# Performance work log

Hardware: AMD Instinct MI355X
Metric: run time of the kernel (lower is better)

## Reference

```python
import jax, jax.numpy as jnp
import numpy as np

N_NODES = 100000
N_EDGES = 640000
D_IN = 128
D_OUT = 128


def setup_inputs() -> dict:
    key = jax.random.key(0)
    k1, k2, k3, k4, k5, k6 = jax.random.split(key, 6)
    x = jax.random.normal(k1, (N_NODES, D_IN), dtype=jnp.float32)
    edge_weights = jax.random.uniform(k2, (N_EDGES, 1), dtype=jnp.float32)
    src = jax.random.randint(k3, (N_EDGES,), 0, N_NODES)
    dst = jax.random.randint(k4, (N_EDGES,), 0, N_NODES)
    # nn.Linear init scale ~ 1/sqrt(in_feats)
    W = jax.random.normal(k5, (D_OUT, D_IN), dtype=jnp.float32) / np.sqrt(D_IN)
    b = jax.random.normal(k6, (D_OUT,), dtype=jnp.float32) / np.sqrt(D_IN)
    return {"x": x, "edge_weights": edge_weights, "src": src, "dst": dst, "W": W, "b": b}


def reference(x, edge_weights, src, dst, W, b):
    # message: gather source node features, scale by per-edge weight  [E, D]
    m = x[src] * edge_weights
    # reduce: sum messages into destination nodes  [N, D]
    h = jax.ops.segment_sum(m, dst, num_segments=N_NODES)
    # dense linear  [N, D_OUT]
    return h @ W.T + b
```

## Files before the change

kernel.cpp:

```cpp
#include <hip/hip_runtime.h>
#include <hip/hip_bf16.h>

#define D 128
#define SCAN_CH 4096
#define HIST_BLOCKS 512

typedef __bf16 bf16x8 __attribute__((ext_vector_type(8)));
typedef float  f32x4  __attribute__((ext_vector_type(4)));
typedef float  f32x2  __attribute__((ext_vector_type(2)));

__device__ __forceinline__ __bf16 f2bf(float f) { return (__bf16)f; }
__device__ __forceinline__ int pad8(int v) { return (v + 7) & ~7; }

__global__ __launch_bounds__(256) void prep_kernel(
    const float* __restrict__ W, __bf16* __restrict__ wb,
    int* __restrict__ cnt, int M, int4* __restrict__ bins4, long nbin4)
{
    long t    = (long)blockIdx.x * 256 + threadIdx.x;
    long nthr = (long)gridDim.x * 256;

    for (long i = t; i < nbin4; i += nthr) bins4[i] = make_int4(0, 0, 0, 0);
    for (long i = t; i < M; i += nthr) cnt[i] = 0;

    if (t < 2048) {
        int lane = (int)t & 63;
        int frag = (int)t >> 6;
        int kb = frag >> 3, fn = frag & 7;
        int n  = fn * 16 + (lane & 15);
        int k0 = kb * 32 + (lane >> 4) * 8;
        const float* src = &W[(size_t)n * D + k0];
        float4 v0 = *reinterpret_cast<const float4*>(src);
        float4 v1 = *reinterpret_cast<const float4*>(src + 4);
        bf16x8 o;
        o[0]=f2bf(v0.x); o[1]=f2bf(v0.y); o[2]=f2bf(v0.z); o[3]=f2bf(v0.w);
        o[4]=f2bf(v1.x); o[5]=f2bf(v1.y); o[6]=f2bf(v1.z); o[7]=f2bf(v1.w);
        *reinterpret_cast<bf16x8*>(&wb[((size_t)frag * 64 + lane) * 8]) = o;
    }
}

__global__ __launch_bounds__(256) void gemm_hist_kernel(
    const float* __restrict__ x, const __bf16* __restrict__ wb,
    __bf16* __restrict__ y, int M,
    const int* __restrict__ dst, int* __restrict__ cnt,
    int* __restrict__ rank, int E)
{
    const int tid = threadIdx.x;

    if (blockIdx.x < HIST_BLOCKS) {
        int t    = blockIdx.x * 256 + tid;
        int nthr = HIST_BLOCKS * 256;
        for (int e = t; e < E; e += nthr) {
            int d = dst[e];
            rank[e] = atomicAdd(&cnt[d], 1);
        }
        return;
    }

    const int gb   = blockIdx.x - HIST_BLOCKS;
    const int lane = tid & 63;
    const int wv   = tid >> 6;
    const int l15  = lane & 15;
    const int l4   = lane >> 4;
    const int row_base = gb * 128 + wv * 32;
    if (row_base >= M) return;

    f32x4 av[2][8];
    #pragma unroll
    for (int mi = 0; mi < 2; ++mi) {
        int row = row_base + mi * 16 + l15;
        int rc  = row < M ? row : M - 1;
        const f32x4* ap = reinterpret_cast<const f32x4*>(&x[(size_t)rc * D + l4 * 8]);
        #pragma unroll
        for (int kb = 0; kb < 4; ++kb) {
            av[mi][kb * 2]     = __builtin_nontemporal_load(ap + kb * 8);
            av[mi][kb * 2 + 1] = __builtin_nontemporal_load(ap + kb * 8 + 1);
        }
    }

    f32x4 acc[2][8];
    #pragma unroll
    for (int mi = 0; mi < 2; ++mi)
        #pragma unroll
        for (int fn = 0; fn < 8; ++fn)
            #pragma unroll
            for (int c = 0; c < 4; ++c) acc[mi][fn][c] = 0.f;

    #pragma unroll
    for (int kb = 0; kb < 4; ++kb) {
        bf16x8 b[8];
        #pragma unroll
        for (int fn = 0; fn < 8; ++fn)
            b[fn] = *reinterpret_cast<const bf16x8*>(
                        &wb[((size_t)(kb * 8 + fn) * 64 + lane) * 8]);
        #pragma unroll
        for (int mi = 0; mi < 2; ++mi) {
            f32x4 v0 = av[mi][kb * 2];
            f32x4 v1 = av[mi][kb * 2 + 1];
            bf16x8 a;
            a[0]=f2bf(v0[0]); a[1]=f2bf(v0[1]); a[2]=f2bf(v0[2]); a[3]=f2bf(v0[3]);
            a[4]=f2bf(v1[0]); a[5]=f2bf(v1[1]); a[6]=f2bf(v1[2]); a[7]=f2bf(v1[3]);
            #pragma unroll
            for (int fn = 0; fn < 8; ++fn)
                acc[mi][fn] = __builtin_amdgcn_mfma_f32_16x16x32_bf16(
                                  a, b[fn], acc[mi][fn], 0, 0, 0);
        }
    }

    #pragma unroll
    for (int mi = 0; mi < 2; ++mi)
        #pragma unroll
        for (int r = 0; r < 4; ++r) {
            int row = row_base + mi * 16 + l4 * 4 + r;
            if (row >= M) continue;
            #pragma unroll
            for (int fn = 0; fn < 8; ++fn)
                y[(size_t)row * D + fn * 16 + l15] = f2bf(acc[mi][fn][r]);
        }
}

__global__ __launch_bounds__(256) void scan_part_kernel(
    const int* __restrict__ cnt, int* __restrict__ bsum, int N)
{
    __shared__ int wred[4];
    const int tid  = threadIdx.x;
    const int lane = tid & 63;
    const int wid  = tid >> 6;
    int off = blockIdx.x * SCAN_CH + tid * 16;
    int s = 0;
    #pragma unroll
    for (int i = 0; i < 16; ++i) {
        int idx = off + i;
        if (idx < N) s += pad8(cnt[idx]);
    }
    #pragma unroll
    for (int d = 32; d >= 1; d >>= 1) s += __shfl_xor(s, d, 64);
    if (lane == 0) wred[wid] = s;
    __syncthreads();
    if (tid == 0) bsum[blockIdx.x] = wred[0] + wred[1] + wred[2] + wred[3];
}

__global__ __launch_bounds__(256) void scan_write_kernel(
    const int* __restrict__ cnt, const int* __restrict__ bsum,
    int* __restrict__ base, int N, int NB)
{
    __shared__ int boff_s;
    __shared__ int wsum[4];
    const int b    = blockIdx.x;
    const int tid  = threadIdx.x;
    const int lane = tid & 63;
    const int wid  = tid >> 6;

    if (wid == 0) {
        int v = (lane < b) ? bsum[lane] : 0;
        #pragma unroll
        for (int d = 32; d >= 1; d >>= 1) v += __shfl_xor(v, d, 64);
        if (lane == 0) boff_s = v;
    }
    __syncthreads();

    int off = b * SCAN_CH + tid * 16;
    int v[16];
    int s = 0;
    #pragma unroll
    for (int i = 0; i < 16; ++i) {
        int idx = off + i;
        v[i] = (idx < N) ? pad8(cnt[idx]) : 0;
        s += v[i];
    }
    int ssum = s;
    #pragma unroll
    for (int d = 1; d < 64; d <<= 1) {
        int t = __shfl_up(ssum, d, 64);
        if (lane >= d) ssum += t;
    }
    if (lane == 63) wsum[wid] = ssum;
    __syncthreads();
    int woff = 0;
    for (int w = 0; w < wid; ++w) woff += wsum[w];

    int run = boff_s + woff + ssum - s;
    #pragma unroll
    for (int i = 0; i < 16; ++i) {
        int idx = off + i;
        if (idx < N) base[idx] = run;
        if (idx == N - 1) base[N] = run + v[i];
        run += v[i];
    }
}

__global__ __launch_bounds__(256) void bin_kernel(
    const int* __restrict__ src, const int* __restrict__ dst,
    const float* __restrict__ ew, const int* __restrict__ base,
    const int* __restrict__ rank, int2* __restrict__ bins, int E)
{
    int e = blockIdx.x * 256 + threadIdx.x;
    if (e >= E) return;
    int d  = __builtin_nontemporal_load(&dst[e]);
    int sv = __builtin_nontemporal_load(&src[e]);
    float w = __builtin_nontemporal_load(&ew[e]);
    int rk = __builtin_nontemporal_load(&rank[e]);
    int p = base[d] + rk;
    bins[p] = make_int2(sv * (D / 2), __float_as_int(w));
}

__global__ __launch_bounds__(256) void gather_kernel(
    const __bf16* __restrict__ y, const int* __restrict__ base,
    const int2* __restrict__ bins, const float* __restrict__ bias,
    float* __restrict__ out, int N)
{
    int gw   = (blockIdx.x * 256 + threadIdx.x) >> 6;
    int lane = threadIdx.x & 63;
    if (gw >= N) return;

    const unsigned* yb = reinterpret_cast<const unsigned*>(y);
    const int b0 = __builtin_amdgcn_readfirstlane(base[gw]);
    const int b1 = __builtin_amdgcn_readfirstlane(base[gw + 1]);
    float accx = 0.f, accy = 0.f;

    for (int i = b0; i < b1; i += 8) {
        int2 e[8];
        #pragma unroll
        for (int t = 0; t < 8; ++t) e[t] = bins[i + t];
        unsigned p[8];
        #pragma unroll
        for (int t = 0; t < 8; ++t)
            p[t] = yb[(unsigned)e[t].x + lane];
        #pragma unroll
        for (int t = 0; t < 8; ++t) {
            float w = __int_as_float(e[t].y);
            accx += __uint_as_float(p[t] << 16) * w;
            accy += __uint_as_float(p[t] & 0xFFFF0000u) * w;
        }
    }

    float2 bv = *reinterpret_cast<const float2*>(&bias[lane * 2]);
    f32x2 o;
    o[0] = accx + bv.x;
    o[1] = accy + bv.y;
    __builtin_nontemporal_store(o, reinterpret_cast<f32x2*>(&out[(size_t)gw * D + lane * 2]));
}

extern "C" void kernel_launch(void* const* d_in, const int* in_sizes, int n_in,
                              void* d_out, int out_size, void* d_ws, size_t ws_size,
                              hipStream_t stream) {
    const float* x   = (const float*)d_in[0];
    const float* ew  = (const float*)d_in[1];
    const int*   src = (const int*)d_in[2];
    const int*   dst = (const int*)d_in[3];
    const float* W   = (const float*)d_in[4];
    const float* b   = (const float*)d_in[5];
    float*       out = (float*)d_out;

    const int E  = in_sizes[2];
    const int M  = out_size / D;
    const int NB = (M + SCAN_CH - 1) / SCAN_CH;
    const size_t BIN_CAP = ((size_t)E + 7 * (size_t)M + 8) & ~(size_t)1;

    char* p = (char*)d_ws;
    __bf16* y    = (__bf16*)p;             p += (size_t)M * D * 2;
    __bf16* wb   = (__bf16*)p;             p += (size_t)32 * 64 * 8 * 2;
    int2*   bins = (int2*)p;               p += BIN_CAP * 8;
    int*    base = (int*)p;                p += (size_t)(M + 1) * 4;
    int*    cnt  = (int*)p;                p += (size_t)M * 4;
    int*    rank = (int*)p;                p += (size_t)E * 4;
    int*    bsum = (int*)p;

    prep_kernel<<<512, 256, 0, stream>>>(W, wb, cnt, M,
                                         (int4*)bins, (long)(BIN_CAP / 2));

    int gemmBlocks = (M + 127) / 128;
    gemm_hist_kernel<<<HIST_BLOCKS + gemmBlocks, 256, 0, stream>>>(
        x, wb, y, M, dst, cnt, rank, E);

    scan_part_kernel<<<NB, 256, 0, stream>>>(cnt, bsum, M);
    scan_write_kernel<<<NB, 256, 0, stream>>>(cnt, bsum, base, M, NB);

    bin_kernel<<<(E + 255) / 256, 256, 0, stream>>>(src, dst, ew, base, rank, bins, E);

    gather_kernel<<<(M * 64 + 255) / 256, 256, 0, stream>>>(y, base, bins, b, out, M);
}
```

Before: 121.6 us.

## Stage GEMM x tile and output through swizzled LDS for coalesced access

The GEMM tile now loads its 128x128 fp32 input tile with fully coalesced 16-byte loads, converts it to bf16 and stores it in a swizzled LDS buffer, and MFMA operands are read back from LDS. The bf16 output is also staged through the same LDS buffer, so each thread writes 16-byte row-contiguous stores instead of scattered 2-byte stores. This targets poor global-memory coalescing on both the x read and the y write. In exchange it adds 32KB of LDS per block and three barriers, which may lower occupancy.

```diff
diff --git a/kernel.cpp b/kernel.cpp
--- a/kernel.cpp
+++ b/kernel.cpp
@@ -6,6 +6,7 @@
 #define HIST_BLOCKS 512
 
 typedef __bf16 bf16x8 __attribute__((ext_vector_type(8)));
+typedef __bf16 bf16x4 __attribute__((ext_vector_type(4)));
 typedef float  f32x4  __attribute__((ext_vector_type(4)));
 typedef float  f32x2  __attribute__((ext_vector_type(2)));
 
@@ -44,6 +45,7 @@
     const int* __restrict__ dst, int* __restrict__ cnt,
     int* __restrict__ rank, int E)
 {
+    __shared__ char xs[128 * 256];
     const int tid = threadIdx.x;
 
     if (blockIdx.x < HIST_BLOCKS) {
@@ -57,25 +59,27 @@
     }
 
     const int gb   = blockIdx.x - HIST_BLOCKS;
+    const int row0 = gb * 128;
     const int lane = tid & 63;
     const int wv   = tid >> 6;
     const int l15  = lane & 15;
     const int l4   = lane >> 4;
-    const int row_base = gb * 128 + wv * 32;
-    if (row_base >= M) return;
-
-    f32x4 av[2][8];
-    #pragma unroll
-    for (int mi = 0; mi < 2; ++mi) {
-        int row = row_base + mi * 16 + l15;
+
+    #pragma unroll
+    for (int i = 0; i < 16; ++i) {
+        int f  = tid + i * 256;
+        int r  = f >> 5;
+        int c8 = f & 31;
+        int row = row0 + r;
         int rc  = row < M ? row : M - 1;
-        const f32x4* ap = reinterpret_cast<const f32x4*>(&x[(size_t)rc * D + l4 * 8]);
-        #pragma unroll
-        for (int kb = 0; kb < 4; ++kb) {
-            av[mi][kb * 2]     = __builtin_nontemporal_load(ap + kb * 8);
-            av[mi][kb * 2 + 1] = __builtin_nontemporal_load(ap + kb * 8 + 1);
-        }
-    }
+        f32x4 v = __builtin_nontemporal_load(
+            reinterpret_cast<const f32x4*>(&x[(size_t)rc * D + c8 * 4]));
+        bf16x4 o;
+        o[0]=f2bf(v[0]); o[1]=f2bf(v[1]); o[2]=f2bf(v[2]); o[3]=f2bf(v[3]);
+        int byte = r * 256 + ((c8 * 8) ^ ((r & 7) << 4));
+        *reinterpret_cast<bf16x4*>(xs + byte) = o;
+    }
+    __syncthreads();
 
     f32x4 acc[2][8];
     #pragma unroll
@@ -94,28 +98,42 @@
                         &wb[((size_t)(kb * 8 + fn) * 64 + lane) * 8]);
         #pragma unroll
         for (int mi = 0; mi < 2; ++mi) {
-            f32x4 v0 = av[mi][kb * 2];
-            f32x4 v1 = av[mi][kb * 2 + 1];
-            bf16x8 a;
-            a[0]=f2bf(v0[0]); a[1]=f2bf(v0[1]); a[2]=f2bf(v0[2]); a[3]=f2bf(v0[3]);
-            a[4]=f2bf(v1[0]); a[5]=f2bf(v1[1]); a[6]=f2bf(v1[2]); a[7]=f2bf(v1[3]);
+            int rl   = wv * 32 + mi * 16 + l15;
+            int byte = rl * 256 + ((kb * 64 + l4 * 16) ^ ((rl & 7) << 4));
+            bf16x8 a = *reinterpret_cast<const bf16x8*>(xs + byte);
             #pragma unroll
             for (int fn = 0; fn < 8; ++fn)
                 acc[mi][fn] = __builtin_amdgcn_mfma_f32_16x16x32_bf16(
                                   a, b[fn], acc[mi][fn], 0, 0, 0);
         }
     }
+    __syncthreads();
 
     #pragma unroll
     for (int mi = 0; mi < 2; ++mi)
         #pragma unroll
         for (int r = 0; r < 4; ++r) {
-            int row = row_base + mi * 16 + l4 * 4 + r;
-            if (row >= M) continue;
+            int rl = wv * 32 + mi * 16 + l4 * 4 + r;
             #pragma unroll
-            for (int fn = 0; fn < 8; ++fn)
-                y[(size_t)row * D + fn * 16 + l15] = f2bf(acc[mi][fn][r]);
-        }
+            for (int fn = 0; fn < 8; ++fn) {
+                int byte = rl * 256 + ((2 * (fn * 16 + l15)) ^ ((rl & 7) << 4));
+                *reinterpret_cast<__bf16*>(xs + byte) = f2bf(acc[mi][fn][r]);
+            }
+        }
+    __syncthreads();
+
+    #pragma unroll
+    for (int i = 0; i < 8; ++i) {
+        int g   = tid + i * 256;
+        int r   = g >> 4;
+        int c16 = g & 15;
+        int row = row0 + r;
+        if (row < M) {
+            int byte = r * 256 + ((c16 * 16) ^ ((r & 7) << 4));
+            bf16x8 v = *reinterpret_cast<const bf16x8*>(xs + byte);
+            *reinterpret_cast<bf16x8*>(&y[(size_t)row * D + c16 * 8]) = v;
+        }
+    }
 }
 
 __global__ __launch_bounds__(256) void scan_part_kernel(
```

After: 121.5 us. No clear change (-0.1%).
